# Optimization experiments

Hardware: AMD Instinct MI355X
Metric: run time of the kernel (lower is better)

The kernel has to match this reference:

```python
import jax, jax.numpy as jnp
import numpy as np

N, E, IN, H, C, L = 40000, 640000, 256, 128, 64, 4
ALPHA, LAMB = 0.5, 1.0


def setup_inputs() -> dict:
    key = jax.random.key(0)
    ks = jax.random.split(key, 8)
    x = jax.random.normal(ks[0], (N, IN), jnp.float32)
    src = jax.random.randint(ks[1], (E,), 0, N, jnp.int32)
    dst = jax.random.randint(ks[2], (E,), 0, N, jnp.int32)
    s_in = 1.0 / np.sqrt(IN)
    s_h = 1.0 / np.sqrt(H)
    fc1_w = jax.random.normal(ks[3], (IN, H), jnp.float32) * s_in
    fc1_b = jnp.zeros((H,), jnp.float32)
    W1 = jax.random.normal(ks[4], (L, H, H), jnp.float32) * s_h   # GCN2Conv weight1 per layer
    W2 = jax.random.normal(ks[5], (L, H, H), jnp.float32) * s_h   # GCN2Conv weight2 (initial-residual proj)
    bgc = jnp.zeros((L, H), jnp.float32)                          # GCN2Conv bias per layer
    fc2_w = jax.random.normal(ks[6], (H, C), jnp.float32) * s_h
    fc2_b = jnp.zeros((C,), jnp.float32)
    return dict(x=x, fc1_w=fc1_w, fc1_b=fc1_b, W1=W1, W2=W2, bgc=bgc,
                fc2_w=fc2_w, fc2_b=fc2_b, src=src, dst=dst)


def reference(x, fc1_w, fc1_b, W1, W2, bgc, fc2_w, fc2_b, src, dst):
    ones = jnp.ones((E,), x.dtype)
    # symmetric 'both' normalization: deg_out^{-1/2} on src side, deg_in^{-1/2} on dst side
    deg_out = jnp.clip(jax.ops.segment_sum(ones, src, num_segments=N), 1.0)
    deg_in = jnp.clip(jax.ops.segment_sum(ones, dst, num_segments=N), 1.0)
    norm_s = (deg_out ** -0.5)[:, None]
    norm_d = (deg_in ** -0.5)[:, None]

    # feature_preprocess: dropout (eval = identity) -> fc1 -> relu
    h0 = jax.nn.relu(x @ fc1_w + fc1_b)          # [N, H]
    h = h0
    for l in range(L):
        beta = float(np.log(LAMB / (l + 1) + 1.0))
        identity = h
        # sparse neighbor aggregation (SpMM via gather + segment_sum)
        agg = jax.ops.segment_sum((h * norm_s)[src], dst, num_segments=N) * norm_d
        feat = (1.0 - ALPHA) * agg               # smoothed features
        f0 = ALPHA * h0                          # initial residual
        rst = (1.0 - beta) * (feat + f0) + beta * (feat @ W1[l] + f0 @ W2[l]) + bgc[l]
        h = jax.nn.relu(rst + identity)          # outer residual + activation (dropout eval = identity)
    return h @ fc2_w + fc2_b                     # [N, C]
```

## Files before the change

kernel.cpp:

```cpp
#include <hip/hip_runtime.h>
#include <math.h>

#define N_NODES 40000
#define N_EDGES 640000
#define IN_F 256
#define H_F 128
#define C_F 64
#define L_LAYERS 4
#define SCAN_BLKS 157
#define N_CHUNKS 64
#define CHUNK_E 10000
#define HIST_WORDS 10000
#define XPAD 264
#define LPAD 132

typedef short short8 __attribute__((ext_vector_type(8)));
typedef unsigned short ushort8 __attribute__((ext_vector_type(8)));
typedef float f32x4 __attribute__((ext_vector_type(4)));

__device__ inline short to_bf16(float f) {
    unsigned u = __builtin_bit_cast(unsigned, f);
    unsigned r = (u + 0x7FFFu + ((u >> 16) & 1u)) >> 16;
    return (short)r;
}
__device__ inline float bf16_to_f(unsigned short u) {
    unsigned v = ((unsigned)u) << 16;
    return __builtin_bit_cast(float, v);
}

__device__ inline int block_excl_scan(int v, int* wsum, int* tot) {
    int tid = threadIdx.x;
    int lane = tid & 63, wid = tid >> 6;
    int incl = v;
    #pragma unroll
    for (int off = 1; off < 64; off <<= 1) {
        int t = __shfl_up(incl, off, 64);
        if (lane >= off) incl += t;
    }
    if (lane == 63) wsum[wid] = incl;
    __syncthreads();
    int prefix = 0, total = 0;
    #pragma unroll
    for (int w = 0; w < 4; w++) {
        int s = wsum[w];
        if (w < wid) prefix += s;
        total += s;
    }
    *tot = total;
    return prefix + incl - v;
}

__global__ __launch_bounds__(256) void prep_fc1w(const float* __restrict__ fc1_w,
                                                 short* __restrict__ fc1_wT) {
    int i = blockIdx.x * 256 + threadIdx.x;
    int n = i >> 8, k = i & 255;
    fc1_wT[i] = to_bf16(fc1_w[k * H_F + n]);
}

__global__ __launch_bounds__(256) void hist_fc1_prep(const int* __restrict__ src,
                                                     const int* __restrict__ dst,
                                                     int* __restrict__ chunk_dst,
                                                     int* __restrict__ chunk_src,
                                                     unsigned char* __restrict__ lrank8,
                                                     const float* __restrict__ x,
                                                     const short* __restrict__ wT,
                                                     const float* __restrict__ b,
                                                     unsigned short* __restrict__ h0b,
                                                     const float* __restrict__ W1,
                                                     const float* __restrict__ W2,
                                                     const float* __restrict__ fc2_w,
                                                     float s0, float s1, float s2, float s3,
                                                     short* __restrict__ WcatT,
                                                     short* __restrict__ fc2_wT) {
    __shared__ union {
        int cntp[HIST_WORDS];
        unsigned short xL[64 * XPAD];
    } sh;
    int blk = blockIdx.x;
    int tid = threadIdx.x;
    if (blk < 128) {
        int role_dst = (blk < 64);
        int w = role_dst ? blk : blk - 64;
        const int* idx = role_dst ? dst : src;
        int base = w * CHUNK_E;
        for (int i = tid; i < HIST_WORDS; i += 256) sh.cntp[i] = 0;
        __syncthreads();
        if (role_dst) {
            for (int i = tid; i < CHUNK_E; i += 256) {
                int d = idx[base + i];
                int shf = (d & 3) * 8;
                int old = atomicAdd(&sh.cntp[d >> 2], 1 << shf);
                lrank8[base + i] = (unsigned char)((old >> shf) & 0xff);
            }
        } else {
            for (int i = tid; i < CHUNK_E; i += 256) {
                int s = idx[base + i];
                atomicAdd(&sh.cntp[s >> 2], 1 << ((s & 3) * 8));
            }
        }
        __syncthreads();
        int* outp = role_dst ? (chunk_dst + w * HIST_WORDS) : (chunk_src + w * HIST_WORDS);
        for (int i = tid; i < HIST_WORDS; i += 256) outp[i] = sh.cntp[i];
        return;
    }
    if (blk >= 753) {
        int i = (blk - 753) * 256 + tid;
        if (i < 4 * 128 * 256) {
            int l = i >> 15; int r = i & 32767; int n = r >> 8; int k = r & 255;
            float sc = (l == 0) ? s0 : (l == 1) ? s1 : (l == 2) ? s2 : s3;
            float w = (k < 128) ? W1[l * 16384 + k * H_F + n]
                                : W2[l * 16384 + (k - 128) * H_F + n];
            WcatT[i] = to_bf16(sc * w);
        }
        if (i < 64 * 128) {
            int n = i >> 7, k = i & 127;
            fc2_wT[i] = to_bf16(fc2_w[k * C_F + n]);
        }
        return;
    }
    int bb = blk - 128;
    const float* xblk = x + (size_t)bb * 64 * IN_F;
    #pragma unroll
    for (int half = 0; half < 2; half++) {
        float4 v[8];
        #pragma unroll
        for (int s = 0; s < 8; s++)
            v[s] = *(const float4*)(xblk + (half * 8 + s) * 1024 + tid * 4);
        #pragma unroll
        for (int s = 0; s < 8; s++) {
            int i = (half * 8 + s) * 1024 + tid * 4;
            int rr = i >> 8, cc = i & 255;
            unsigned p0 = (unsigned)(unsigned short)to_bf16(v[s].x)
                        | ((unsigned)(unsigned short)to_bf16(v[s].y) << 16);
            unsigned p1 = (unsigned)(unsigned short)to_bf16(v[s].z)
                        | ((unsigned)(unsigned short)to_bf16(v[s].w) << 16);
            uint2 pk = {p0, p1};
            *(uint2*)(sh.xL + rr * XPAD + cc) = pk;
        }
    }
    __syncthreads();
    int wave = tid >> 6, lane = tid & 63;
    int m = lane & 15, quad = lane >> 4;
    const unsigned short* xr = sh.xL + (wave * 16 + m) * XPAD + quad * 8;
    short8 afrag[8];
    #pragma unroll
    for (int ks = 0; ks < 8; ks++) {
        afrag[ks] = __builtin_bit_cast(short8, *(const ushort8*)(xr + ks * 32));
    }
    #pragma unroll
    for (int c = 0; c < 8; c += 2) {
        f32x4 acc0 = {0.f, 0.f, 0.f, 0.f};
        f32x4 acc1 = {0.f, 0.f, 0.f, 0.f};
        const short* b0p = wT + (size_t)(c * 16 + m) * IN_F + quad * 8;
        const short* b1p = b0p + 16 * IN_F;
        #pragma unroll
        for (int ks = 0; ks < 8; ks++) {
            short8 b0 = *(const short8*)(b0p + ks * 32);
            short8 b1 = *(const short8*)(b1p + ks * 32);
            acc0 = __builtin_amdgcn_mfma_f32_16x16x32_bf16(afrag[ks], b0, acc0, 0, 0, 0);
            acc1 = __builtin_amdgcn_mfma_f32_16x16x32_bf16(afrag[ks], b1, acc1, 0, 0, 0);
        }
        int col0 = c * 16 + m;
        int rbase = bb * 64 + wave * 16 + quad * 4;
        float bg0 = b[col0], bg1 = b[col0 + 16];
        #pragma unroll
        for (int r = 0; r < 4; r++) {
            size_t idx2 = (size_t)(rbase + r) * H_F + col0;
            float v0 = acc0[r] + bg0;
            float v1 = acc1[r] + bg1;
            v0 = v0 > 0.f ? v0 : 0.f;
            v1 = v1 > 0.f ? v1 : 0.f;
            h0b[idx2] = (unsigned short)to_bf16(v0);
            h0b[idx2 + 16] = (unsigned short)to_bf16(v1);
        }
    }
}

__global__ __launch_bounds__(256) void scan1(const int* __restrict__ chunk_dst,
                                             const int* __restrict__ chunk_src,
                                             int* __restrict__ base32,
                                             float* __restrict__ rsq_in,
                                             float* __restrict__ rsq_out,
                                             float* __restrict__ sq_out,
                                             int* __restrict__ row_local,
                                             int* __restrict__ blk_sum) {
    __shared__ int wsum[4];
    int sb = blockIdx.x;
    int n = sb * 256 + threadIdx.x;
    int deg = 0, word = 0, sh = 0;
    if (n < N_NODES) {
        word = n >> 2; sh = (n & 3) * 8;
        #pragma unroll 4
        for (int w = 0; w < N_CHUNKS; w++)
            deg += (chunk_dst[w * HIST_WORDS + word] >> sh) & 0xff;
    }
    int tot;
    int excl = block_excl_scan(deg, wsum, &tot);
    if (n < N_NODES) {
        row_local[n] = excl;
        int run = excl;
        #pragma unroll 4
        for (int w = 0; w < N_CHUNKS; w++) {
            int v = (chunk_dst[w * HIST_WORDS + word] >> sh) & 0xff;
            base32[(size_t)w * N_NODES + n] = run;
            run += v;
        }
        int so = 0;
        #pragma unroll 4
        for (int w = 0; w < N_CHUNKS; w++)
            so += (chunk_src[w * HIST_WORDS + word] >> sh) & 0xff;
        float fd = (float)(deg < 1 ? 1 : deg);
        float fs = (float)(so < 1 ? 1 : so);
        rsq_in[n] = 1.0f / sqrtf(fd);
        rsq_out[n] = 1.0f / sqrtf(fs);
        sq_out[n] = sqrtf(fs);
    }
    if (threadIdx.x == 0) blk_sum[sb] = tot;
}

__global__ __launch_bounds__(256) void fill_fused(const int* __restrict__ src,
                                                  const int* __restrict__ dst,
                                                  const unsigned char* __restrict__ lrank8,
                                                  const int* __restrict__ base32,
                                                  const int* __restrict__ row_local,
                                                  const int* __restrict__ blk_sum,
                                                  unsigned short* __restrict__ col16,
                                                  int* __restrict__ row_ptr,
                                                  const unsigned short* __restrict__ h0b,
                                                  const float* __restrict__ rsq_out,
                                                  unsigned short* __restrict__ h0s) {
    __shared__ int wsum[4];
    __shared__ int blk_offL[SCAN_BLKS];
    int tid = threadIdx.x;
    {
        int v = (tid < SCAN_BLKS) ? blk_sum[tid] : 0;
        int tot;
        int excl = block_excl_scan(v, wsum, &tot);
        if (tid < SCAN_BLKS) blk_offL[tid] = excl;
    }
    __syncthreads();

    int blk = blockIdx.x;
    if (blk < 2500) {
        int e = blk * 256 + tid;
        int w = e / CHUNK_E;
        int s = src[e], d = dst[e];
        int rp = blk_offL[d >> 8] + base32[(size_t)w * N_NODES + d] + (int)lrank8[e];
        col16[rp] = (unsigned short)s;
        return;
    }
    if (blk < 2657) {
        int n = (blk - 2500) * 256 + tid;
        if (n < N_NODES) row_ptr[n] = blk_offL[n >> 8] + row_local[n];
        if (blk == 2500 && tid == 0) row_ptr[N_NODES] = N_EDGES;
        return;
    }
    int j = (blk - 2657) * 2048 + tid * 8;
    ushort8 u = *(const ushort8*)(h0b + j);
    float rs = rsq_out[j >> 7];
    ushort8 o;
    #pragma unroll
    for (int jj = 0; jj < 8; jj++) o[jj] = (unsigned short)to_bf16(rs * bf16_to_f(u[jj]));
    *(ushort8*)(h0s + j) = o;
}

__global__ __launch_bounds__(256) void layer_fused(const unsigned short* __restrict__ hs_in,
                                                   const unsigned short* __restrict__ h0b,
                                                   const int* __restrict__ row_ptr,
                                                   const unsigned short* __restrict__ col16,
                                                   const float* __restrict__ rsq_in,
                                                   const float* __restrict__ rsq_out,
                                                   const float* __restrict__ sq_out,
                                                   const short* __restrict__ wT,
                                                   const float* __restrict__ bgc,
                                                   float omb5,
                                                   unsigned short* __restrict__ hs_out,
                                                   const short* __restrict__ fc2_wT,
                                                   const float* __restrict__ fc2_b,
                                                   float* __restrict__ out) {
    __shared__ unsigned short aggL[16 * LPAD];
    __shared__ unsigned short vL[16 * LPAD];
    int tid = threadIdx.x;
    int wave = tid >> 6, lane = tid & 63;
    int slot = lane >> 4, fi = lane & 15;
    int nodebase = blockIdx.x * 16;

    #pragma unroll
    for (int i = 0; i < 4; i++) {
        int rl = wave * 4 + i;
        int n = nodebase + rl;
        int e0 = row_ptr[n], e1 = row_ptr[n + 1];
        float a[8] = {};
        for (int e = e0 + slot; e < e1; e += 16) {
            int eb = e + 4, ec = e + 8, ed = e + 12;
            int c0 = col16[e];
            int c1 = (eb < e1) ? col16[eb] : c0;  float w1 = (eb < e1) ? 1.f : 0.f;
            int c2 = (ec < e1) ? col16[ec] : c0;  float w2 = (ec < e1) ? 1.f : 0.f;
            int c3 = (ed < e1) ? col16[ed] : c0;  float w3 = (ed < e1) ? 1.f : 0.f;
            ushort8 u0 = *(const ushort8*)(hs_in + (size_t)c0 * H_F + fi * 8);
            ushort8 u1 = *(const ushort8*)(hs_in + (size_t)c1 * H_F + fi * 8);
            ushort8 u2 = *(const ushort8*)(hs_in + (size_t)c2 * H_F + fi * 8);
            ushort8 u3 = *(const ushort8*)(hs_in + (size_t)c3 * H_F + fi * 8);
            #pragma unroll
            for (int j = 0; j < 8; j++) {
                a[j] += bf16_to_f(u0[j]) + w1 * bf16_to_f(u1[j])
                      + w2 * bf16_to_f(u2[j]) + w3 * bf16_to_f(u3[j]);
            }
        }
        #pragma unroll
        for (int mask = 16; mask <= 32; mask <<= 1) {
            #pragma unroll
            for (int j = 0; j < 8; j++) a[j] += __shfl_xor(a[j], mask, 64);
        }
        if (slot == 0) {
            float rs = rsq_in[n];
            ushort8 r;
            #pragma unroll
            for (int j = 0; j < 8; j++) r[j] = (unsigned short)to_bf16(rs * a[j]);
            *(ushort8*)(aggL + rl * LPAD + fi * 8) = r;
        }
    }
    __syncthreads();

    int m = lane & 15, quad = lane >> 4;
    {
        const unsigned short* aggr = aggL + m * LPAD + quad * 8;
        const unsigned short* h0r  = h0b + (size_t)(nodebase + m) * H_F + quad * 8;
        short8 afrag[8];
        #pragma unroll
        for (int ks = 0; ks < 4; ks++) {
            afrag[ks] = __builtin_bit_cast(short8, *(const ushort8*)(aggr + ks * 32));
            afrag[ks + 4] = __builtin_bit_cast(short8, *(const ushort8*)(h0r + ks * 32));
        }
        int c = wave * 2;
        f32x4 acc0 = {0.f, 0.f, 0.f, 0.f};
        f32x4 acc1 = {0.f, 0.f, 0.f, 0.f};
        const short* b0p = wT + (size_t)(c * 16 + m) * 256 + quad * 8;
        const short* b1p = b0p + 16 * 256;
        #pragma unroll
        for (int ks = 0; ks < 8; ks++) {
            short8 b0 = *(const short8*)(b0p + ks * 32);
            short8 b1 = *(const short8*)(b1p + ks * 32);
            acc0 = __builtin_amdgcn_mfma_f32_16x16x32_bf16(afrag[ks], b0, acc0, 0, 0, 0);
            acc1 = __builtin_amdgcn_mfma_f32_16x16x32_bf16(afrag[ks], b1, acc1, 0, 0, 0);
        }
        int col0 = c * 16 + m;
        float bg0 = bgc[col0], bg1 = bgc[col0 + 16];
        #pragma unroll
        for (int r = 0; r < 4; r++) {
            int rl = quad * 4 + r;
            int rw = nodebase + rl;
            size_t idx = (size_t)rw * H_F + col0;
            float sq = sq_out[rw];
            float rsq = rsq_out[rw];
            float s0 = bf16_to_f(aggL[rl * LPAD + col0]) + bf16_to_f(h0b[idx]);
            float s1 = bf16_to_f(aggL[rl * LPAD + col0 + 16]) + bf16_to_f(h0b[idx + 16]);
            float v0 = omb5 * s0 + acc0[r] + bg0 + sq * bf16_to_f(hs_in[idx]);
            float v1 = omb5 * s1 + acc1[r] + bg1 + sq * bf16_to_f(hs_in[idx + 16]);
            v0 = v0 > 0.f ? v0 : 0.f;
            v1 = v1 > 0.f ? v1 : 0.f;
            hs_out[idx] = (unsigned short)to_bf16(rsq * v0);
            hs_out[idx + 16] = (unsigned short)to_bf16(rsq * v1);
            if (out) {
                vL[rl * LPAD + col0] = (unsigned short)to_bf16(v0);
                vL[rl * LPAD + col0 + 16] = (unsigned short)to_bf16(v1);
            }
        }
    }

    if (out) {
        __syncthreads();
        const unsigned short* vr = vL + m * LPAD + quad * 8;
        short8 afrag[4];
        #pragma unroll
        for (int ks = 0; ks < 4; ks++) {
            afrag[ks] = __builtin_bit_cast(short8, *(const ushort8*)(vr + ks * 32));
        }
        int c = wave;
        f32x4 acc = {0.f, 0.f, 0.f, 0.f};
        const short* bp = fc2_wT + (size_t)(c * 16 + m) * H_F + quad * 8;
        #pragma unroll
        for (int ks = 0; ks < 4; ks++) {
            short8 b0 = *(const short8*)(bp + ks * 32);
            acc = __builtin_amdgcn_mfma_f32_16x16x32_bf16(afrag[ks], b0, acc, 0, 0, 0);
        }
        int col0 = c * 16 + m;
        float bg = fc2_b[col0];
        #pragma unroll
        for (int r = 0; r < 4; r++) {
            int rw = nodebase + quad * 4 + r;
            out[(size_t)rw * C_F + col0] = acc[r] + bg;
        }
    }
}

extern "C" void kernel_launch(void* const* d_in, const int* in_sizes, int n_in,
                              void* d_out, int out_size, void* d_ws, size_t ws_size,
                              hipStream_t stream) {
    const float* x     = (const float*)d_in[0];
    const float* fc1_w = (const float*)d_in[1];
    const float* fc1_b = (const float*)d_in[2];
    const float* W1    = (const float*)d_in[3];
    const float* W2    = (const float*)d_in[4];
    const float* bgc   = (const float*)d_in[5];
    const float* fc2_w = (const float*)d_in[6];
    const float* fc2_b = (const float*)d_in[7];
    const int*   src   = (const int*)d_in[8];
    const int*   dst   = (const int*)d_in[9];
    float* out = (float*)d_out;

    char* p = (char*)d_ws;
    auto alloc = [&](size_t bytes) {
        char* r = p;
        p += (bytes + 255) & ~(size_t)255;
        return r;
    };
    int*   chunk_dst = (int*)alloc((size_t)N_CHUNKS * HIST_WORDS * 4);
    int*   chunk_src = (int*)alloc((size_t)N_CHUNKS * HIST_WORDS * 4);
    int*   base32    = (int*)alloc((size_t)N_CHUNKS * N_NODES * 4);
    unsigned char* lrank8 = (unsigned char*)alloc((size_t)N_EDGES);
    float* rsq_in  = (float*)alloc((size_t)N_NODES * 4);
    float* rsq_out = (float*)alloc((size_t)N_NODES * 4);
    float* sq_out  = (float*)alloc((size_t)N_NODES * 4);
    int*   row_ptr   = (int*)alloc((size_t)(N_NODES + 1) * 4);
    int*   row_local = (int*)alloc((size_t)N_NODES * 4);
    int*   blk_sum   = (int*)alloc((size_t)SCAN_BLKS * 4);
    unsigned short* col16 = (unsigned short*)alloc((size_t)N_EDGES * 2);
    unsigned short* h0b  = (unsigned short*)alloc((size_t)N_NODES * H_F * 2);
    unsigned short* h0s  = (unsigned short*)alloc((size_t)N_NODES * H_F * 2);
    unsigned short* hAs  = (unsigned short*)alloc((size_t)N_NODES * H_F * 2);
    unsigned short* hBs  = (unsigned short*)alloc((size_t)N_NODES * H_F * 2);
    short* fc1_wT  = (short*)alloc((size_t)128 * 256 * 2);
    short* WcatT   = (short*)alloc((size_t)4 * 128 * 256 * 2);
    short* fc2_wT  = (short*)alloc((size_t)64 * 128 * 2);

    float beta[4], wscale[4], omb5[4];
    for (int l = 0; l < 4; l++) {
        beta[l] = (float)log(1.0 / (double)(l + 1) + 1.0);
        wscale[l] = 0.5f * beta[l];
        omb5[l] = 0.5f * (1.f - beta[l]);
    }

    prep_fc1w<<<128, 256, 0, stream>>>(fc1_w, fc1_wT);
    hist_fc1_prep<<<1265, 256, 0, stream>>>(src, dst, chunk_dst, chunk_src, lrank8,
                                            x, fc1_wT, fc1_b, h0b,
                                            W1, W2, fc2_w,
                                            wscale[0], wscale[1], wscale[2], wscale[3],
                                            WcatT, fc2_wT);
    scan1<<<SCAN_BLKS, 256, 0, stream>>>(chunk_dst, chunk_src, base32,
                                         rsq_in, rsq_out, sq_out, row_local, blk_sum);
    fill_fused<<<5157, 256, 0, stream>>>(src, dst, lrank8, base32, row_local, blk_sum,
                                         col16, row_ptr, h0b, rsq_out, h0s);

    const unsigned short* sp_in[4] = {h0s, hAs, hBs, hAs};
    unsigned short* out_b[4]       = {hAs, hBs, hAs, hBs};
    for (int l = 0; l < L_LAYERS; l++) {
        int last = (l == L_LAYERS - 1);
        layer_fused<<<N_NODES / 16, 256, 0, stream>>>(sp_in[l], h0b, row_ptr, col16,
                                                      rsq_in, rsq_out, sq_out,
                                                      WcatT + (size_t)l * 128 * 256,
                                                      bgc + (size_t)l * H_F,
                                                      omb5[l], out_b[l],
                                                      last ? fc2_wT : (const short*)nullptr,
                                                      last ? fc2_b : (const float*)nullptr,
                                                      last ? out : (float*)nullptr);
    }
}
```

Before: 359.0 us.

## Gather neighbor features from an FP8 copy in SpMM aggregation

Each layer now also writes an FP8 (e4m3) copy of the scaled hidden state, and the neighbor gather in the aggregation reads 16 bytes of FP8 per lane instead of bf16. This halves the bytes pulled through the random-access gather, which is the dominant memory cost. Lanes are remapped to 8 slots of 8 lanes covering 16 features each, with a wider shuffle reduction. It adds an extra pass and block sync to pack FP8 output, and FP8 rounding lowers accuracy of the aggregated features, which risks exceeding tolerance.

```diff
diff --git a/kernel.cpp b/kernel.cpp
--- a/kernel.cpp
+++ b/kernel.cpp
@@ -17,6 +17,7 @@
 typedef short short8 __attribute__((ext_vector_type(8)));
 typedef unsigned short ushort8 __attribute__((ext_vector_type(8)));
 typedef float f32x4 __attribute__((ext_vector_type(4)));
+typedef float f32x2 __attribute__((ext_vector_type(2)));
 
 __device__ inline short to_bf16(float f) {
     unsigned u = __builtin_bit_cast(unsigned, f);
@@ -26,6 +27,24 @@
 __device__ inline float bf16_to_f(unsigned short u) {
     unsigned v = ((unsigned)u) << 16;
     return __builtin_bit_cast(float, v);
+}
+__device__ inline unsigned pack_fp8x4(float v0, float v1, float v2, float v3) {
+    int r = 0;
+    r = __builtin_amdgcn_cvt_pk_fp8_f32(v0, v1, r, false);
+    r = __builtin_amdgcn_cvt_pk_fp8_f32(v2, v3, r, true);
+    return (unsigned)r;
+}
+__device__ inline void acc_fp8x16(float* a, uint4 u, float wgt) {
+    unsigned uu[4] = {u.x, u.y, u.z, u.w};
+    #pragma unroll
+    for (int q = 0; q < 4; q++) {
+        f32x2 lo = __builtin_amdgcn_cvt_pk_f32_fp8((int)uu[q], false);
+        f32x2 hi = __builtin_amdgcn_cvt_pk_f32_fp8((int)uu[q], true);
+        a[q * 4 + 0] += wgt * lo[0];
+        a[q * 4 + 1] += wgt * lo[1];
+        a[q * 4 + 2] += wgt * hi[0];
+        a[q * 4 + 3] += wgt * hi[1];
+    }
 }
 
 __device__ inline int block_excl_scan(int v, int* wsum, int* tot) {
@@ -228,7 +247,8 @@
                                                   int* __restrict__ row_ptr,
                                                   const unsigned short* __restrict__ h0b,
                                                   const float* __restrict__ rsq_out,
-                                                  unsigned short* __restrict__ h0s) {
+                                                  unsigned short* __restrict__ h0s,
+                                                  unsigned char* __restrict__ h0f8) {
     __shared__ int wsum[4];
     __shared__ int blk_offL[SCAN_BLKS];
     int tid = threadIdx.x;
@@ -258,13 +278,20 @@
     int j = (blk - 2657) * 2048 + tid * 8;
     ushort8 u = *(const ushort8*)(h0b + j);
     float rs = rsq_out[j >> 7];
+    float f[8];
     ushort8 o;
     #pragma unroll
-    for (int jj = 0; jj < 8; jj++) o[jj] = (unsigned short)to_bf16(rs * bf16_to_f(u[jj]));
+    for (int jj = 0; jj < 8; jj++) {
+        f[jj] = rs * bf16_to_f(u[jj]);
+        o[jj] = (unsigned short)to_bf16(f[jj]);
+    }
     *(ushort8*)(h0s + j) = o;
+    uint2 pk = {pack_fp8x4(f[0], f[1], f[2], f[3]), pack_fp8x4(f[4], f[5], f[6], f[7])};
+    *(uint2*)(h0f8 + j) = pk;
 }
 
 __global__ __launch_bounds__(256) void layer_fused(const unsigned short* __restrict__ hs_in,
+                                                   const unsigned char* __restrict__ hf8_in,
                                                    const unsigned short* __restrict__ h0b,
                                                    const int* __restrict__ row_ptr,
                                                    const unsigned short* __restrict__ col16,
@@ -275,6 +302,7 @@
                                                    const float* __restrict__ bgc,
                                                    float omb5,
                                                    unsigned short* __restrict__ hs_out,
+                                                   unsigned char* __restrict__ hf8_out,
                                                    const short* __restrict__ fc2_wT,
                                                    const float* __restrict__ fc2_b,
                                                    float* __restrict__ out) {
@@ -282,7 +310,7 @@
     __shared__ unsigned short vL[16 * LPAD];
     int tid = threadIdx.x;
     int wave = tid >> 6, lane = tid & 63;
-    int slot = lane >> 4, fi = lane & 15;
+    int slot = lane >> 3, fi = lane & 7;
     int nodebase = blockIdx.x * 16;
 
     #pragma unroll
@@ -290,34 +318,37 @@
         int rl = wave * 4 + i;
         int n = nodebase + rl;
         int e0 = row_ptr[n], e1 = row_ptr[n + 1];
-        float a[8] = {};
-        for (int e = e0 + slot; e < e1; e += 16) {
-            int eb = e + 4, ec = e + 8, ed = e + 12;
+        float a[16] = {};
+        for (int e = e0 + slot; e < e1; e += 32) {
+            int eb = e + 8, ec = e + 16, ed = e + 24;
             int c0 = col16[e];
             int c1 = (eb < e1) ? col16[eb] : c0;  float w1 = (eb < e1) ? 1.f : 0.f;
             int c2 = (ec < e1) ? col16[ec] : c0;  float w2 = (ec < e1) ? 1.f : 0.f;
             int c3 = (ed < e1) ? col16[ed] : c0;  float w3 = (ed < e1) ? 1.f : 0.f;
-            ushort8 u0 = *(const ushort8*)(hs_in + (size_t)c0 * H_F + fi * 8);
-            ushort8 u1 = *(const ushort8*)(hs_in + (size_t)c1 * H_F + fi * 8);
-            ushort8 u2 = *(const ushort8*)(hs_in + (size_t)c2 * H_F + fi * 8);
-            ushort8 u3 = *(const ushort8*)(hs_in + (size_t)c3 * H_F + fi * 8);
+            uint4 u0 = *(const uint4*)(hf8_in + (size_t)c0 * H_F + fi * 16);
+            uint4 u1 = *(const uint4*)(hf8_in + (size_t)c1 * H_F + fi * 16);
+            uint4 u2 = *(const uint4*)(hf8_in + (size_t)c2 * H_F + fi * 16);
+            uint4 u3 = *(const uint4*)(hf8_in + (size_t)c3 * H_F + fi * 16);
+            acc_fp8x16(a, u0, 1.f);
+            acc_fp8x16(a, u1, w1);
+            acc_fp8x16(a, u2, w2);
+            acc_fp8x16(a, u3, w3);
+        }
+        #pragma unroll
+        for (int mask = 8; mask <= 32; mask <<= 1) {
+            #pragma unroll
+            for (int j = 0; j < 16; j++) a[j] += __shfl_xor(a[j], mask, 64);
+        }
+        if (slot == 0) {
+            float rs = rsq_in[n];
+            ushort8 r0, r1;
             #pragma unroll
             for (int j = 0; j < 8; j++) {
-                a[j] += bf16_to_f(u0[j]) + w1 * bf16_to_f(u1[j])
-                      + w2 * bf16_to_f(u2[j]) + w3 * bf16_to_f(u3[j]);
+                r0[j] = (unsigned short)to_bf16(rs * a[j]);
+                r1[j] = (unsigned short)to_bf16(rs * a[j + 8]);
             }
-        }
-        #pragma unroll
-        for (int mask = 16; mask <= 32; mask <<= 1) {
-            #pragma unroll
-            for (int j = 0; j < 8; j++) a[j] += __shfl_xor(a[j], mask, 64);
-        }
-        if (slot == 0) {
-            float rs = rsq_in[n];
-            ushort8 r;
-            #pragma unroll
-            for (int j = 0; j < 8; j++) r[j] = (unsigned short)to_bf16(rs * a[j]);
-            *(ushort8*)(aggL + rl * LPAD + fi * 8) = r;
+            *(ushort8*)(aggL + rl * LPAD + fi * 16) = r0;
+            *(ushort8*)(aggL + rl * LPAD + fi * 16 + 8) = r1;
         }
     }
     __syncthreads();
@@ -359,17 +390,33 @@
             float v1 = omb5 * s1 + acc1[r] + bg1 + sq * bf16_to_f(hs_in[idx + 16]);
             v0 = v0 > 0.f ? v0 : 0.f;
             v1 = v1 > 0.f ? v1 : 0.f;
-            hs_out[idx] = (unsigned short)to_bf16(rsq * v0);
-            hs_out[idx + 16] = (unsigned short)to_bf16(rsq * v1);
+            unsigned short b16a = (unsigned short)to_bf16(rsq * v0);
+            unsigned short b16b = (unsigned short)to_bf16(rsq * v1);
+            hs_out[idx] = b16a;
+            hs_out[idx + 16] = b16b;
             if (out) {
                 vL[rl * LPAD + col0] = (unsigned short)to_bf16(v0);
                 vL[rl * LPAD + col0 + 16] = (unsigned short)to_bf16(v1);
+            } else {
+                vL[rl * LPAD + col0] = b16a;
+                vL[rl * LPAD + col0 + 16] = b16b;
             }
         }
     }
+    __syncthreads();
+
+    if (hf8_out) {
+        int row = tid >> 4, fb = (tid & 15) * 8;
+        const unsigned short* vr = vL + row * LPAD + fb;
+        float f[8];
+        #pragma unroll
+        for (int j = 0; j < 8; j++) f[j] = bf16_to_f(vr[j]);
+        uint2 pk = {pack_fp8x4(f[0], f[1], f[2], f[3]),
+                    pack_fp8x4(f[4], f[5], f[6], f[7])};
+        *(uint2*)(hf8_out + (size_t)(nodebase + row) * H_F + fb) = pk;
+    }
 
     if (out) {
-        __syncthreads();
         const unsigned short* vr = vL + m * LPAD + quad * 8;
         short8 afrag[4];
         #pragma unroll
@@ -430,6 +477,9 @@
     unsigned short* h0s  = (unsigned short*)alloc((size_t)N_NODES * H_F * 2);
     unsigned short* hAs  = (unsigned short*)alloc((size_t)N_NODES * H_F * 2);
     unsigned short* hBs  = (unsigned short*)alloc((size_t)N_NODES * H_F * 2);
+    unsigned char* h0f8  = (unsigned char*)alloc((size_t)N_NODES * H_F);
+    unsigned char* hAf8  = (unsigned char*)alloc((size_t)N_NODES * H_F);
+    unsigned char* hBf8  = (unsigned char*)alloc((size_t)N_NODES * H_F);
     short* fc1_wT  = (short*)alloc((size_t)128 * 256 * 2);
     short* WcatT   = (short*)alloc((size_t)4 * 128 * 256 * 2);
     short* fc2_wT  = (short*)alloc((size_t)64 * 128 * 2);
@@ -450,17 +500,20 @@
     scan1<<<SCAN_BLKS, 256, 0, stream>>>(chunk_dst, chunk_src, base32,
                                          rsq_in, rsq_out, sq_out, row_local, blk_sum);
     fill_fused<<<5157, 256, 0, stream>>>(src, dst, lrank8, base32, row_local, blk_sum,
-                                         col16, row_ptr, h0b, rsq_out, h0s);
+                                         col16, row_ptr, h0b, rsq_out, h0s, h0f8);
 
     const unsigned short* sp_in[4] = {h0s, hAs, hBs, hAs};
+    const unsigned char*  f8_in[4] = {h0f8, hAf8, hBf8, hAf8};
     unsigned short* out_b[4]       = {hAs, hBs, hAs, hBs};
+    unsigned char*  out_f8[4]      = {hAf8, hBf8, hAf8, nullptr};
     for (int l = 0; l < L_LAYERS; l++) {
         int last = (l == L_LAYERS - 1);
-        layer_fused<<<N_NODES / 16, 256, 0, stream>>>(sp_in[l], h0b, row_ptr, col16,
+        layer_fused<<<N_NODES / 16, 256, 0, stream>>>(sp_in[l], f8_in[l], h0b,
+                                                      row_ptr, col16,
                                                       rsq_in, rsq_out, sq_out,
                                                       WcatT + (size_t)l * 128 * 256,
                                                       bgc + (size_t)l * H_F,
-                                                      omb5[l], out_b[l],
+                                                      omb5[l], out_b[l], out_f8[l],
                                                       last ? fc2_wT : (const short*)nullptr,
                                                       last ? fc2_b : (const float*)nullptr,
                                                       last ? out : (float*)nullptr);
```

Result: slower. 379.1 us (+5.6%).

## Group nodes by in-degree via a permutation to balance layer workloads

Applied to the files above, without the earlier changes.

Adds a degree histogram in scan1 and a new perm_build kernel that buckets nodes by in-degree (capped at 63) into a permutation. Each layer block then processes 16 nodes of similar degree, so the waves in a block carry similar aggregation loads and per-block imbalance shrinks. In exchange, output and h0 rows are written and read through an indirection, which scatters accesses that used to be contiguous, and the preprocessing gains an extra kernel plus atomics. The memset clears dhist and cursor together, which relies on cursor being allocated directly after dhist.

```diff
diff --git a/kernel.cpp b/kernel.cpp
--- a/kernel.cpp
+++ b/kernel.cpp
@@ -13,6 +13,7 @@
 #define HIST_WORDS 10000
 #define XPAD 264
 #define LPAD 132
+#define DBINS 64
 
 typedef short short8 __attribute__((ext_vector_type(8)));
 typedef unsigned short ushort8 __attribute__((ext_vector_type(8)));
@@ -183,10 +184,15 @@
                                              float* __restrict__ rsq_out,
                                              float* __restrict__ sq_out,
                                              int* __restrict__ row_local,
-                                             int* __restrict__ blk_sum) {
+                                             int* __restrict__ blk_sum,
+                                             unsigned short* __restrict__ deg16,
+                                             int* __restrict__ dhist) {
     __shared__ int wsum[4];
+    __shared__ int lhist[DBINS];
+    int tid = threadIdx.x;
+    if (tid < DBINS) lhist[tid] = 0;
     int sb = blockIdx.x;
-    int n = sb * 256 + threadIdx.x;
+    int n = sb * 256 + tid;
     int deg = 0, word = 0, sh = 0;
     if (n < N_NODES) {
         word = n >> 2; sh = (n & 3) * 8;
@@ -214,8 +220,32 @@
         rsq_in[n] = 1.0f / sqrtf(fd);
         rsq_out[n] = 1.0f / sqrtf(fs);
         sq_out[n] = sqrtf(fs);
-    }
-    if (threadIdx.x == 0) blk_sum[sb] = tot;
+        int db = deg < (DBINS - 1) ? deg : (DBINS - 1);
+        deg16[n] = (unsigned short)db;
+        atomicAdd(&lhist[db], 1);
+    }
+    if (tid == 0) blk_sum[sb] = tot;
+    __syncthreads();
+    if (tid < DBINS && lhist[tid]) atomicAdd(&dhist[tid], lhist[tid]);
+}
+
+__global__ __launch_bounds__(256) void perm_build(const unsigned short* __restrict__ deg16,
+                                                  const int* __restrict__ dhist,
+                                                  int* __restrict__ cursor,
+                                                  int* __restrict__ perm) {
+    __shared__ int baseL[DBINS];
+    int tid = threadIdx.x;
+    if (tid == 0) {
+        int run = 0;
+        for (int i = 0; i < DBINS; i++) { baseL[i] = run; run += dhist[i]; }
+    }
+    __syncthreads();
+    int n = blockIdx.x * 256 + tid;
+    if (n < N_NODES) {
+        int d = deg16[n];
+        int pos = baseL[d] + atomicAdd(&cursor[d], 1);
+        perm[pos] = n;
+    }
 }
 
 __global__ __launch_bounds__(256) void fill_fused(const int* __restrict__ src,
@@ -268,6 +298,7 @@
                                                    const unsigned short* __restrict__ h0b,
                                                    const int* __restrict__ row_ptr,
                                                    const unsigned short* __restrict__ col16,
+                                                   const int* __restrict__ perm,
                                                    const float* __restrict__ rsq_in,
                                                    const float* __restrict__ rsq_out,
                                                    const float* __restrict__ sq_out,
@@ -280,15 +311,18 @@
                                                    float* __restrict__ out) {
     __shared__ unsigned short aggL[16 * LPAD];
     __shared__ unsigned short vL[16 * LPAD];
+    __shared__ int nodeL[16];
     int tid = threadIdx.x;
     int wave = tid >> 6, lane = tid & 63;
     int slot = lane >> 4, fi = lane & 15;
     int nodebase = blockIdx.x * 16;
+    if (tid < 16) nodeL[tid] = perm[nodebase + tid];
+    __syncthreads();
 
     #pragma unroll
     for (int i = 0; i < 4; i++) {
         int rl = wave * 4 + i;
-        int n = nodebase + rl;
+        int n = nodeL[rl];
         int e0 = row_ptr[n], e1 = row_ptr[n + 1];
         float a[8] = {};
         for (int e = e0 + slot; e < e1; e += 16) {
@@ -324,8 +358,9 @@
 
     int m = lane & 15, quad = lane >> 4;
     {
+        int nm = nodeL[m];
         const unsigned short* aggr = aggL + m * LPAD + quad * 8;
-        const unsigned short* h0r  = h0b + (size_t)(nodebase + m) * H_F + quad * 8;
+        const unsigned short* h0r  = h0b + (size_t)nm * H_F + quad * 8;
         short8 afrag[8];
         #pragma unroll
         for (int ks = 0; ks < 4; ks++) {
@@ -349,7 +384,7 @@
         #pragma unroll
         for (int r = 0; r < 4; r++) {
             int rl = quad * 4 + r;
-            int rw = nodebase + rl;
+            int rw = nodeL[rl];
             size_t idx = (size_t)rw * H_F + col0;
             float sq = sq_out[rw];
             float rsq = rsq_out[rw];
@@ -388,7 +423,7 @@
         float bg = fc2_b[col0];
         #pragma unroll
         for (int r = 0; r < 4; r++) {
-            int rw = nodebase + quad * 4 + r;
+            int rw = nodeL[quad * 4 + r];
             out[(size_t)rw * C_F + col0] = acc[r] + bg;
         }
     }
@@ -425,6 +460,10 @@
     int*   row_ptr   = (int*)alloc((size_t)(N_NODES + 1) * 4);
     int*   row_local = (int*)alloc((size_t)N_NODES * 4);
     int*   blk_sum   = (int*)alloc((size_t)SCAN_BLKS * 4);
+    unsigned short* deg16 = (unsigned short*)alloc((size_t)N_NODES * 2);
+    int*   dhist   = (int*)alloc((size_t)DBINS * 4);
+    int*   cursor  = (int*)alloc((size_t)DBINS * 4);
+    int*   perm    = (int*)alloc((size_t)N_NODES * 4);
     unsigned short* col16 = (unsigned short*)alloc((size_t)N_EDGES * 2);
     unsigned short* h0b  = (unsigned short*)alloc((size_t)N_NODES * H_F * 2);
     unsigned short* h0s  = (unsigned short*)alloc((size_t)N_NODES * H_F * 2);
@@ -441,6 +480,8 @@
         omb5[l] = 0.5f * (1.f - beta[l]);
     }
 
+    hipMemsetAsync(dhist, 0, DBINS * 8, stream);
+
     prep_fc1w<<<128, 256, 0, stream>>>(fc1_w, fc1_wT);
     hist_fc1_prep<<<1265, 256, 0, stream>>>(src, dst, chunk_dst, chunk_src, lrank8,
                                             x, fc1_wT, fc1_b, h0b,
@@ -448,7 +489,9 @@
                                             wscale[0], wscale[1], wscale[2], wscale[3],
                                             WcatT, fc2_wT);
     scan1<<<SCAN_BLKS, 256, 0, stream>>>(chunk_dst, chunk_src, base32,
-                                         rsq_in, rsq_out, sq_out, row_local, blk_sum);
+                                         rsq_in, rsq_out, sq_out, row_local, blk_sum,
+                                         deg16, dhist);
+    perm_build<<<SCAN_BLKS, 256, 0, stream>>>(deg16, dhist, cursor, perm);
     fill_fused<<<5157, 256, 0, stream>>>(src, dst, lrank8, base32, row_local, blk_sum,
                                          col16, row_ptr, h0b, rsq_out, h0s);
 
@@ -457,7 +500,7 @@
     for (int l = 0; l < L_LAYERS; l++) {
         int last = (l == L_LAYERS - 1);
         layer_fused<<<N_NODES / 16, 256, 0, stream>>>(sp_in[l], h0b, row_ptr, col16,
-                                                      rsq_in, rsq_out, sq_out,
+                                                      perm, rsq_in, rsq_out, sq_out,
                                                       WcatT + (size_t)l * 128 * 256,
                                                       bgc + (size_t)l * H_F,
                                                       omb5[l], out_b[l],
```

Result: slower. 474.8 us (+32.2%).
